# Kernel optimization log

Hardware: AMD Instinct MI355X
Metric: run time of the kernel (lower is better)

The kernel has to match this reference:

```python
import jax, jax.numpy as jnp
import numpy as np

EPS = 1e-8  # torch CosineSimilarity eps


def _l2_normalize(x):
    n = jnp.sqrt(jnp.sum(x * x, axis=-1, keepdims=True))
    return x / jnp.maximum(n, EPS)


def setup_inputs() -> dict:
    key = jax.random.key(0)
    k1, k2, k3 = jax.random.split(key, 3)
    B, D, K = 4096, 1024, 256
    datapoints = jax.random.normal(k1, (B, D), dtype=jnp.float32)
    centroid = jax.random.normal(k2, (K, D), dtype=jnp.float32)
    batch_cos_sim = jax.random.normal(k3, (B, B), dtype=jnp.float32)
    return {"datapoints": datapoints, "centroid": centroid, "batch_cos_sim": batch_cos_sim}


def reference(datapoints, centroid, batch_cos_sim):
    # --- _clustering: cosine similarity datapoints[B,D] vs centroid[K,D] (temp=1) ---
    dn = _l2_normalize(datapoints)                       # [B, D]
    cn = _l2_normalize(centroid)                         # [K, D]
    intra_cos_sim = jnp.einsum('bd,kd->bk', dn, cn)      # [B, K]
    dp_index = jnp.argmax(intra_cos_sim, axis=-1)        # [B]

    # --- _intra_class_adjacency: one-hot matmul, zero diagonal ---
    onehot = jax.nn.one_hot(dp_index, centroid.shape[0], dtype=jnp.float32)  # [B, K]
    dp_cluster = jnp.einsum('bk,ck->bc', onehot, onehot)                      # [B, B]
    B = datapoints.shape[0]
    dp_cluster = dp_cluster * (1.0 - jnp.eye(B, dtype=dp_cluster.dtype))
    index_dp = onehot.T.astype(jnp.int32)                # [K, B]

    # --- gather centroid each datapoint belongs to ---
    dp_centroid = centroid[dp_index]                     # [B, D]

    # --- provide_hard_negative: top-2, take 2nd-best centroid ---
    top_vals, top_idx = jax.lax.top_k(intra_cos_sim, 2)  # [B, 2]
    hard_neg_index = top_idx[:, 1]                       # [B]
    hard_negative = centroid[hard_neg_index]             # [B, D]

    return (intra_cos_sim, dp_index, dp_cluster, index_dp, dp_centroid,
            hard_negative, hard_neg_index, top_vals[:, 1])
```

## Files before the change

kernel.cpp:

```cpp
#include <hip/hip_runtime.h>
#include <hip/hip_bf16.h>
#include <math.h>

#define B_N 4096
#define D_N 1024
#define K_N 256
#define NSTEP 32

typedef __attribute__((ext_vector_type(8))) short bf16x8;
typedef __attribute__((ext_vector_type(8))) unsigned short u16x8;
typedef __attribute__((ext_vector_type(4))) float f32x4;
typedef __attribute__((ext_vector_type(4))) float f32x4v;
typedef __attribute__((ext_vector_type(4))) int   i32x4;

static constexpr float K_EPS = 1e-8f;

static __device__ __forceinline__ unsigned short f32_to_bf16_rne(float f) {
    unsigned x = __builtin_bit_cast(unsigned, f);
    unsigned r = (x + 0x7FFFu + ((x >> 16) & 1u)) >> 16;
    return (unsigned short)r;
}
static __device__ __forceinline__ float bf16_bits_to_f32(unsigned short h) {
    unsigned x = ((unsigned)h) << 16;
    return __builtin_bit_cast(float, x);
}
static __device__ __forceinline__ void cvt8(
    float e0, float e1, float e2, float e3,
    float e4, float e5, float e6, float e7, u16x8& hv, u16x8& lv)
{
    ushort h0=f32_to_bf16_rne(e0), h1=f32_to_bf16_rne(e1),
           h2=f32_to_bf16_rne(e2), h3=f32_to_bf16_rne(e3),
           h4=f32_to_bf16_rne(e4), h5=f32_to_bf16_rne(e5),
           h6=f32_to_bf16_rne(e6), h7=f32_to_bf16_rne(e7);
    hv = (u16x8){h0,h1,h2,h3,h4,h5,h6,h7};
    lv = (u16x8){f32_to_bf16_rne(e0 - bf16_bits_to_f32(h0)),
                 f32_to_bf16_rne(e1 - bf16_bits_to_f32(h1)),
                 f32_to_bf16_rne(e2 - bf16_bits_to_f32(h2)),
                 f32_to_bf16_rne(e3 - bf16_bits_to_f32(h3)),
                 f32_to_bf16_rne(e4 - bf16_bits_to_f32(h4)),
                 f32_to_bf16_rne(e5 - bf16_bits_to_f32(h5)),
                 f32_to_bf16_rne(e6 - bf16_bits_to_f32(h6)),
                 f32_to_bf16_rne(e7 - bf16_bits_to_f32(h7))};
}

__global__ __launch_bounds__(256) void kcent_kernel(
    const float* __restrict__ cent,
    ushort* __restrict__ phi, ushort* __restrict__ plo)
{
    int n   = blockIdx.x;
    int tid = threadIdx.x;
    float4 v = reinterpret_cast<const float4*>(cent + (size_t)n * D_N)[tid];
    float s = v.x * v.x + v.y * v.y + v.z * v.z + v.w * v.w;
    #pragma unroll
    for (int o = 32; o > 0; o >>= 1) s += __shfl_down(s, o);
    __shared__ float red[4];
    __shared__ float s_inv;
    if ((tid & 63) == 0) red[tid >> 6] = s;
    __syncthreads();
    if (tid == 0) {
        float t = red[0] + red[1] + red[2] + red[3];
        s_inv = 1.0f / fmaxf(sqrtf(t), K_EPS);
    }
    __syncthreads();
    float inv = s_inv;
    float e[4] = {v.x * inv, v.y * inv, v.z * inv, v.w * inv};
    ushort h4[4], l4[4];
    #pragma unroll
    for (int j = 0; j < 4; ++j) {
        ushort h = f32_to_bf16_rne(e[j]);
        float lo = e[j] - bf16_bits_to_f32(h);
        h4[j] = h;
        l4[j] = f32_to_bf16_rne(lo);
    }
    int nt = n >> 4, lr = n & 15;
    int k8 = tid >> 1, half = tid & 1;
    int t  = k8 >> 2, lg = k8 & 3;
    size_t chunk = (size_t)(nt * 32 + t) * 64 + lg * 16 + lr;
    *reinterpret_cast<ushort4*>(phi + chunk * 8 + half * 4) =
        make_ushort4(h4[0], h4[1], h4[2], h4[3]);
    *reinterpret_cast<ushort4*>(plo + chunk * 8 + half * 4) =
        make_ushort4(l4[0], l4[1], l4[2], l4[3]);
}

__global__ __launch_bounds__(1024) void kmain_kernel(
    const float* __restrict__ dp, const float* __restrict__ cent,
    const ushort* __restrict__ phi, const ushort* __restrict__ plo,
    float* __restrict__ out_sims, float* __restrict__ out_dpidx,
    float* __restrict__ out_hnidx, float* __restrict__ out_top1,
    float* __restrict__ out_dpcent, float* __restrict__ out_hneg,
    int* __restrict__ ws_dpidx)
{
    __shared__ ushort AhL[32 * 1024];
    __shared__ ushort AlL[32 * 1024];
    float* simsL = (float*)AhL;
    int tid  = threadIdx.x;
    int lane = tid & 63;
    int w    = tid >> 6;
    int lr   = lane & 15;
    int lg   = lane >> 4;
    int brow = blockIdx.x * 32;

    const ushort* bh = phi + (size_t)w * 32 * 512 + (size_t)lane * 8;
    const ushort* bl = plo + (size_t)w * 32 * 512 + (size_t)lane * 8;

    #define LBF(t, H, L)                                                  \
        H = *reinterpret_cast<const bf16x8*>(bh + (size_t)(t) * 512);     \
        L = *reinterpret_cast<const bf16x8*>(bl + (size_t)(t) * 512);

    bf16x8 h0,l0,h1,l1,h2,l2,h3,l3,h4,l4,h5,l5,h6,l6,h7,l7;
    LBF(0,h0,l0) LBF(1,h1,l1) LBF(2,h2,l2) LBF(3,h3,l3)
    LBF(4,h4,l4) LBF(5,h5,l5) LBF(6,h6,l6) LBF(7,h7,l7)

    #pragma unroll
    for (int rloc = 0; rloc < 2; ++rloc) {
        int row_l = w * 2 + rloc;
        const f32x4v* r4 = reinterpret_cast<const f32x4v*>(
            dp + (size_t)(brow + row_l) * D_N);
        f32x4v a0 = __builtin_nontemporal_load(r4 + lane*4+0);
        f32x4v a1 = __builtin_nontemporal_load(r4 + lane*4+1);
        f32x4v a2 = __builtin_nontemporal_load(r4 + lane*4+2);
        f32x4v a3 = __builtin_nontemporal_load(r4 + lane*4+3);
        float s = a0[0]*a0[0] + a0[1]*a0[1] + a0[2]*a0[2] + a0[3]*a0[3]
                + a1[0]*a1[0] + a1[1]*a1[1] + a1[2]*a1[2] + a1[3]*a1[3]
                + a2[0]*a2[0] + a2[1]*a2[1] + a2[2]*a2[2] + a2[3]*a2[3]
                + a3[0]*a3[0] + a3[1]*a3[1] + a3[2]*a3[2] + a3[3]*a3[3];
        #pragma unroll
        for (int o = 1; o < 64; o <<= 1) s += __shfl_xor(s, o);
        float inv = 1.0f / fmaxf(sqrtf(s), K_EPS);
        u16x8 hv, lv;
        cvt8(a0[0]*inv, a0[1]*inv, a0[2]*inv, a0[3]*inv,
             a1[0]*inv, a1[1]*inv, a1[2]*inv, a1[3]*inv, hv, lv);
        int slot = (lane*2 + 0) ^ (row_l & 7);
        *reinterpret_cast<u16x8*>(&AhL[row_l*1024 + slot*8]) = hv;
        *reinterpret_cast<u16x8*>(&AlL[row_l*1024 + slot*8]) = lv;
        cvt8(a2[0]*inv, a2[1]*inv, a2[2]*inv, a2[3]*inv,
             a3[0]*inv, a3[1]*inv, a3[2]*inv, a3[3]*inv, hv, lv);
        slot = (lane*2 + 1) ^ (row_l & 7);
        *reinterpret_cast<u16x8*>(&AhL[row_l*1024 + slot*8]) = hv;
        *reinterpret_cast<u16x8*>(&AlL[row_l*1024 + slot*8]) = lv;
    }
    __syncthreads();

    f32x4 acc0 = {}, acc1 = {};
    const char* AhC = (const char*)AhL;
    const char* AlC = (const char*)AlL;
    auto step = [&](int t, bf16x8 hb, bf16x8 lb) {
        unsigned ca = (unsigned)((4*t + lg) ^ (lr & 7));
        unsigned ao0 = (unsigned)lr * 2048u + ca * 16u;
        unsigned ao1 = (unsigned)(16 + lr) * 2048u + ca * 16u;
        bf16x8 ah0 = *reinterpret_cast<const bf16x8*>(AhC + ao0);
        bf16x8 al0 = *reinterpret_cast<const bf16x8*>(AlC + ao0);
        bf16x8 ah1 = *reinterpret_cast<const bf16x8*>(AhC + ao1);
        bf16x8 al1 = *reinterpret_cast<const bf16x8*>(AlC + ao1);
        acc0 = __builtin_amdgcn_mfma_f32_16x16x32_bf16(ah0, hb, acc0, 0, 0, 0);
        acc0 = __builtin_amdgcn_mfma_f32_16x16x32_bf16(ah0, lb, acc0, 0, 0, 0);
        acc0 = __builtin_amdgcn_mfma_f32_16x16x32_bf16(al0, hb, acc0, 0, 0, 0);
        acc1 = __builtin_amdgcn_mfma_f32_16x16x32_bf16(ah1, hb, acc1, 0, 0, 0);
        acc1 = __builtin_amdgcn_mfma_f32_16x16x32_bf16(ah1, lb, acc1, 0, 0, 0);
        acc1 = __builtin_amdgcn_mfma_f32_16x16x32_bf16(al1, hb, acc1, 0, 0, 0);
    };
    #pragma unroll 1
    for (int t = 0; t < NSTEP; t += 8) {
        step(t + 0, h0, l0); if (t +  8 < NSTEP) { LBF(t +  8, h0, l0) }
        step(t + 1, h1, l1); if (t +  9 < NSTEP) { LBF(t +  9, h1, l1) }
        step(t + 2, h2, l2); if (t + 10 < NSTEP) { LBF(t + 10, h2, l2) }
        step(t + 3, h3, l3); if (t + 11 < NSTEP) { LBF(t + 11, h3, l3) }
        step(t + 4, h4, l4); if (t + 12 < NSTEP) { LBF(t + 12, h4, l4) }
        step(t + 5, h5, l5); if (t + 13 < NSTEP) { LBF(t + 13, h5, l5) }
        step(t + 6, h6, l6); if (t + 14 < NSTEP) { LBF(t + 14, h6, l6) }
        step(t + 7, h7, l7); if (t + 15 < NSTEP) { LBF(t + 15, h7, l7) }
    }
    #undef LBF

    __syncthreads();
    #pragma unroll
    for (int r = 0; r < 4; ++r) {
        simsL[(lg*4 + r) * K_N + w*16 + lr]        = acc0[r];
        simsL[(16 + lg*4 + r) * K_N + w*16 + lr]   = acc1[r];
    }
    __syncthreads();

    #pragma unroll
    for (int rloc = 0; rloc < 2; ++rloc) {
        int row_l = w * 2 + rloc;
        int row   = brow + row_l;
        f32x4v c = *reinterpret_cast<const f32x4v*>(&simsL[row_l * K_N + lane * 4]);
        __builtin_nontemporal_store(c,
            reinterpret_cast<f32x4v*>(&out_sims[(size_t)row * K_N + lane * 4]));
        float v1b = c[0]; int i1 = lane * 4;
        float v2b = -INFINITY; int i2 = 0;
        {
            float vals[3] = {c[1], c[2], c[3]};
            #pragma unroll
            for (int j = 0; j < 3; ++j) {
                float val = vals[j]; int idx = lane * 4 + j + 1;
                if (val > v1b) { v2b = v1b; i2 = i1; v1b = val; i1 = idx; }
                else if (val > v2b) { v2b = val; i2 = idx; }
            }
        }
        #pragma unroll
        for (int o = 1; o < 64; o <<= 1) {
            float ov1 = __shfl_xor(v1b, o);
            float ov2 = __shfl_xor(v2b, o);
            int   oi1 = __shfl_xor(i1, o);
            int   oi2 = __shfl_xor(i2, o);
            if (ov1 > v1b || (ov1 == v1b && oi1 < i1)) {
                float nv2; int ni2;
                if (v1b > ov2 || (v1b == ov2 && i1 < oi2)) { nv2 = v1b; ni2 = i1; }
                else { nv2 = ov2; ni2 = oi2; }
                v1b = ov1; i1 = oi1; v2b = nv2; i2 = ni2;
            } else if (ov1 > v2b || (ov1 == v2b && oi1 < i2)) {
                v2b = ov1; i2 = oi1;
            }
        }
        const f32x4v* cent4 = reinterpret_cast<const f32x4v*>(cent);
        #pragma unroll
        for (int q = 0; q < 4; ++q) {
            f32x4v g1 = cent4[(size_t)i1 * 256 + q * 64 + lane];
            f32x4v g2 = cent4[(size_t)i2 * 256 + q * 64 + lane];
            __builtin_nontemporal_store(g1,
                reinterpret_cast<f32x4v*>(out_dpcent + (size_t)row * D_N) + q*64 + lane);
            __builtin_nontemporal_store(g2,
                reinterpret_cast<f32x4v*>(out_hneg + (size_t)row * D_N) + q*64 + lane);
        }
        if (lane == 0) {
            out_dpidx[row] = (float)i1;
            out_hnidx[row] = (float)i2;
            out_top1[row]  = v2b;
            ws_dpidx[row]  = i1;
        }
    }
}

__global__ __launch_bounds__(256) void kclust_kernel(
    const int* __restrict__ dpidx,
    float* __restrict__ out_cluster, float* __restrict__ out_indexdp)
{
    int bid = blockIdx.x;
    int tid = threadIdx.x;
    const i32x4* dpi4 = reinterpret_cast<const i32x4*>(dpidx);
    if (bid < B_N) {
        int i = bid;
        int me = dpidx[i];
        float* dst = out_cluster + (size_t)i * B_N;
        #pragma unroll
        for (int q = 0; q < 4; ++q) {
            int j = q * 1024 + tid * 4;
            i32x4 ix = dpi4[j >> 2];
            f32x4v v;
            v[0] = (ix[0] == me && (j + 0) != i) ? 1.0f : 0.0f;
            v[1] = (ix[1] == me && (j + 1) != i) ? 1.0f : 0.0f;
            v[2] = (ix[2] == me && (j + 2) != i) ? 1.0f : 0.0f;
            v[3] = (ix[3] == me && (j + 3) != i) ? 1.0f : 0.0f;
            __builtin_nontemporal_store(v, reinterpret_cast<f32x4v*>(dst + j));
        }
    } else {
        int k = bid - B_N;
        float* dst = out_indexdp + (size_t)k * B_N;
        #pragma unroll
        for (int q = 0; q < 4; ++q) {
            int j = q * 1024 + tid * 4;
            i32x4 ix = dpi4[j >> 2];
            f32x4v v;
            v[0] = (ix[0] == k) ? 1.0f : 0.0f;
            v[1] = (ix[1] == k) ? 1.0f : 0.0f;
            v[2] = (ix[2] == k) ? 1.0f : 0.0f;
            v[3] = (ix[3] == k) ? 1.0f : 0.0f;
            __builtin_nontemporal_store(v, reinterpret_cast<f32x4v*>(dst + j));
        }
    }
}

extern "C" void kernel_launch(void* const* d_in, const int* in_sizes, int n_in,
                              void* d_out, int out_size, void* d_ws, size_t ws_size,
                              hipStream_t stream)
{
    const float* dp   = (const float*)d_in[0];
    const float* cent = (const float*)d_in[1];
    float* out = (float*)d_out;

    float* o_sims   = out;
    float* o_dpidx  = out + 1048576;
    float* o_clust  = out + 1052672;
    float* o_idxdp  = out + 17829888;
    float* o_dpcent = out + 18878464;
    float* o_hneg   = out + 23072768;
    float* o_hnidx  = out + 27267072;
    float* o_top1   = out + 27271168;

    char* ws = (char*)d_ws;
    ushort* phi  = (ushort*)ws;
    ushort* plo  = (ushort*)(ws + (512u << 10));
    int*    widx = (int*)(ws + (1u << 20));

    hipLaunchKernelGGL(kcent_kernel, dim3(K_N), dim3(256), 0, stream,
                       cent, phi, plo);
    hipLaunchKernelGGL(kmain_kernel, dim3(B_N / 32), dim3(1024), 0, stream,
                       dp, cent, phi, plo,
                       o_sims, o_dpidx, o_hnidx, o_top1,
                       o_dpcent, o_hneg, widx);
    hipLaunchKernelGGL(kclust_kernel, dim3(B_N + K_N), dim3(256), 0, stream,
                       widx, o_clust, o_idxdp);
}
```

Baseline: 49.47 us.

## Retile main kernel to 16 rows per block with two column tiles per wave

The main kernel now processes 16 datapoint rows per block with 512 threads (8 waves) instead of 32 rows with 1024 threads, and each wave computes two 16-column centroid tiles instead of two row tiles. Grid size doubles to 256 blocks, which fills more of the CUs and halves the shared memory per block, allowing several blocks per CU. In exchange, every block rereads the full centroid matrix from global/L2, doubling the centroid traffic, and the prefetch depth drops from 8 steps to 2.

```diff
diff --git a/kernel.cpp b/kernel.cpp
--- a/kernel.cpp
+++ b/kernel.cpp
@@ -82,7 +82,7 @@
         make_ushort4(l4[0], l4[1], l4[2], l4[3]);
 }
 
-__global__ __launch_bounds__(1024) void kmain_kernel(
+__global__ __launch_bounds__(512, 4) void kmain_kernel(
     const float* __restrict__ dp, const float* __restrict__ cent,
     const ushort* __restrict__ phi, const ushort* __restrict__ plo,
     float* __restrict__ out_sims, float* __restrict__ out_dpidx,
@@ -90,26 +90,30 @@
     float* __restrict__ out_dpcent, float* __restrict__ out_hneg,
     int* __restrict__ ws_dpidx)
 {
-    __shared__ ushort AhL[32 * 1024];
-    __shared__ ushort AlL[32 * 1024];
+    __shared__ ushort AhL[16 * 1024];
+    __shared__ ushort AlL[16 * 1024];
     float* simsL = (float*)AhL;
     int tid  = threadIdx.x;
     int lane = tid & 63;
     int w    = tid >> 6;
     int lr   = lane & 15;
     int lg   = lane >> 4;
-    int brow = blockIdx.x * 32;
-
-    const ushort* bh = phi + (size_t)w * 32 * 512 + (size_t)lane * 8;
-    const ushort* bl = plo + (size_t)w * 32 * 512 + (size_t)lane * 8;
-
-    #define LBF(t, H, L)                                                  \
-        H = *reinterpret_cast<const bf16x8*>(bh + (size_t)(t) * 512);     \
-        L = *reinterpret_cast<const bf16x8*>(bl + (size_t)(t) * 512);
-
-    bf16x8 h0,l0,h1,l1,h2,l2,h3,l3,h4,l4,h5,l5,h6,l6,h7,l7;
-    LBF(0,h0,l0) LBF(1,h1,l1) LBF(2,h2,l2) LBF(3,h3,l3)
-    LBF(4,h4,l4) LBF(5,h5,l5) LBF(6,h6,l6) LBF(7,h7,l7)
+    int brow = blockIdx.x * 16;
+
+    const ushort* bh0 = phi + (size_t)(w * 2) * 16384 + (size_t)lane * 8;
+    const ushort* bl0 = plo + (size_t)(w * 2) * 16384 + (size_t)lane * 8;
+    const ushort* bh1 = bh0 + 16384;
+    const ushort* bl1 = bl0 + 16384;
+
+    #define LBF(t, H0, L0, H1, L1)                                        \
+        H0 = *reinterpret_cast<const bf16x8*>(bh0 + (size_t)(t) * 512);   \
+        L0 = *reinterpret_cast<const bf16x8*>(bl0 + (size_t)(t) * 512);   \
+        H1 = *reinterpret_cast<const bf16x8*>(bh1 + (size_t)(t) * 512);   \
+        L1 = *reinterpret_cast<const bf16x8*>(bl1 + (size_t)(t) * 512);
+
+    bf16x8 p0h0,p0l0,p0h1,p0l1, p1h0,p1l0,p1h1,p1l1;
+    LBF(0, p0h0,p0l0,p0h1,p0l1)
+    LBF(1, p1h0,p1l0,p1h1,p1l1)
 
     #pragma unroll
     for (int rloc = 0; rloc < 2; ++rloc) {
@@ -144,39 +148,32 @@
     f32x4 acc0 = {}, acc1 = {};
     const char* AhC = (const char*)AhL;
     const char* AlC = (const char*)AlL;
-    auto step = [&](int t, bf16x8 hb, bf16x8 lb) {
+    auto step = [&](int t, bf16x8 h0, bf16x8 l0, bf16x8 h1, bf16x8 l1) {
         unsigned ca = (unsigned)((4*t + lg) ^ (lr & 7));
-        unsigned ao0 = (unsigned)lr * 2048u + ca * 16u;
-        unsigned ao1 = (unsigned)(16 + lr) * 2048u + ca * 16u;
-        bf16x8 ah0 = *reinterpret_cast<const bf16x8*>(AhC + ao0);
-        bf16x8 al0 = *reinterpret_cast<const bf16x8*>(AlC + ao0);
-        bf16x8 ah1 = *reinterpret_cast<const bf16x8*>(AhC + ao1);
-        bf16x8 al1 = *reinterpret_cast<const bf16x8*>(AlC + ao1);
-        acc0 = __builtin_amdgcn_mfma_f32_16x16x32_bf16(ah0, hb, acc0, 0, 0, 0);
-        acc0 = __builtin_amdgcn_mfma_f32_16x16x32_bf16(ah0, lb, acc0, 0, 0, 0);
-        acc0 = __builtin_amdgcn_mfma_f32_16x16x32_bf16(al0, hb, acc0, 0, 0, 0);
-        acc1 = __builtin_amdgcn_mfma_f32_16x16x32_bf16(ah1, hb, acc1, 0, 0, 0);
-        acc1 = __builtin_amdgcn_mfma_f32_16x16x32_bf16(ah1, lb, acc1, 0, 0, 0);
-        acc1 = __builtin_amdgcn_mfma_f32_16x16x32_bf16(al1, hb, acc1, 0, 0, 0);
+        unsigned ao = (unsigned)lr * 2048u + ca * 16u;
+        bf16x8 ah = *reinterpret_cast<const bf16x8*>(AhC + ao);
+        bf16x8 al = *reinterpret_cast<const bf16x8*>(AlC + ao);
+        acc0 = __builtin_amdgcn_mfma_f32_16x16x32_bf16(ah, h0, acc0, 0, 0, 0);
+        acc0 = __builtin_amdgcn_mfma_f32_16x16x32_bf16(ah, l0, acc0, 0, 0, 0);
+        acc0 = __builtin_amdgcn_mfma_f32_16x16x32_bf16(al, h0, acc0, 0, 0, 0);
+        acc1 = __builtin_amdgcn_mfma_f32_16x16x32_bf16(ah, h1, acc1, 0, 0, 0);
+        acc1 = __builtin_amdgcn_mfma_f32_16x16x32_bf16(ah, l1, acc1, 0, 0, 0);
+        acc1 = __builtin_amdgcn_mfma_f32_16x16x32_bf16(al, h1, acc1, 0, 0, 0);
     };
     #pragma unroll 1
-    for (int t = 0; t < NSTEP; t += 8) {
-        step(t + 0, h0, l0); if (t +  8 < NSTEP) { LBF(t +  8, h0, l0) }
-        step(t + 1, h1, l1); if (t +  9 < NSTEP) { LBF(t +  9, h1, l1) }
-        step(t + 2, h2, l2); if (t + 10 < NSTEP) { LBF(t + 10, h2, l2) }
-        step(t + 3, h3, l3); if (t + 11 < NSTEP) { LBF(t + 11, h3, l3) }
-        step(t + 4, h4, l4); if (t + 12 < NSTEP) { LBF(t + 12, h4, l4) }
-        step(t + 5, h5, l5); if (t + 13 < NSTEP) { LBF(t + 13, h5, l5) }
-        step(t + 6, h6, l6); if (t + 14 < NSTEP) { LBF(t + 14, h6, l6) }
-        step(t + 7, h7, l7); if (t + 15 < NSTEP) { LBF(t + 15, h7, l7) }
+    for (int t = 0; t < NSTEP; t += 2) {
+        step(t, p0h0, p0l0, p0h1, p0l1);
+        if (t + 2 < NSTEP) { LBF(t + 2, p0h0, p0l0, p0h1, p0l1) }
+        step(t + 1, p1h0, p1l0, p1h1, p1l1);
+        if (t + 3 < NSTEP) { LBF(t + 3, p1h0, p1l0, p1h1, p1l1) }
     }
     #undef LBF
 
     __syncthreads();
     #pragma unroll
     for (int r = 0; r < 4; ++r) {
-        simsL[(lg*4 + r) * K_N + w*16 + lr]        = acc0[r];
-        simsL[(16 + lg*4 + r) * K_N + w*16 + lr]   = acc1[r];
+        simsL[(lg*4 + r) * K_N + (w*2 + 0)*16 + lr] = acc0[r];
+        simsL[(lg*4 + r) * K_N + (w*2 + 1)*16 + lr] = acc1[r];
     }
     __syncthreads();
 
@@ -295,7 +292,7 @@
 
     hipLaunchKernelGGL(kcent_kernel, dim3(K_N), dim3(256), 0, stream,
                        cent, phi, plo);
-    hipLaunchKernelGGL(kmain_kernel, dim3(B_N / 32), dim3(1024), 0, stream,
+    hipLaunchKernelGGL(kmain_kernel, dim3(B_N / 16), dim3(512), 0, stream,
                        dp, cent, phi, plo,
                        o_sims, o_dpidx, o_hnidx, o_top1,
                        o_dpcent, o_hneg, widx);
```

Measured after the change: 45.68 us. 7.7% less time.
